# Performance work log

Hardware: AMD Instinct MI355X
Metric: run time of the kernel (lower is better)

The kernel has to match this reference:

```python
import jax, jax.numpy as jnp
import numpy as np

B, C = 8388608, 4
OTHERS_IDX = 3

def setup_inputs() -> dict:
    key = jax.random.key(0)
    k1, k2 = jax.random.split(key)
    preds = jax.random.normal(k1, (B, C), dtype=jnp.float32)
    target = jax.random.randint(k2, (B,), 0, C, dtype=jnp.int64)
    return {"preds": preds, "target": target, "others_idx": OTHERS_IDX}

def reference(preds, target, others_idx):
    # softmax over class dim (dim=1 in the torch module)
    probs = jax.nn.softmax(preds, axis=1)              # [B, C]
    p_o = probs[:, others_idx]                          # [B]
    s = probs.sum(axis=1)                               # [B] (== 1, but computed as in original)
    # per-sample false-negative error (samples whose target IS the 'others' class)
    fne_i = 0.5 * ((s - p_o) ** 2 + (p_o - 1.0) ** 2)   # [B]
    # per-sample false-positive error (samples whose target is NOT 'others')
    fpe_i = 0.5 * ((-p_o) ** 2 + p_o ** 2)              # [B]
    is_others = (target == others_idx)                  # [B] bool
    fne_num = jnp.sum(is_others).astype(probs.dtype)
    fpe_num = jnp.sum(~is_others).astype(probs.dtype)
    fne = jnp.sum(jnp.where(is_others, fne_i, 0.0)) / fne_num
    fpe = jnp.sum(jnp.where(is_others, 0.0, fpe_i)) / fpe_num
    return fpe + fne
```

## Files before the change

### kernel.cpp

```cpp
#include <hip/hip_runtime.h>


#define BLOCK 256
#define ROWS 16

__device__ __forceinline__ void mfe_row(float4 x, int t, int o,
                                        float& fne_acc, float& fpe_acc,
                                        float& cnt_acc) {
    float m = fmaxf(fmaxf(x.x, x.y), fmaxf(x.z, x.w));
    float e0 = __expf(x.x - m);
    float e1 = __expf(x.y - m);
    float e2 = __expf(x.z - m);
    float e3 = __expf(x.w - m);
    float S = (e0 + e1) + (e2 + e3);
    float r = 1.0f / S;
    float p0 = e0 * r, p1 = e1 * r, p2 = e2 * r, p3 = e3 * r;
    float s = ((p0 + p1) + p2) + p3;
    float po = (o == 0) ? p0 : (o == 1) ? p1 : (o == 2) ? p2 : p3;

    float d1 = s - po;
    float d2 = po - 1.0f;
    float fne_i = 0.5f * (d1 * d1 + d2 * d2);
    float fpe_i = po * po;

    bool is_o = (t == o);
    fne_acc += is_o ? fne_i : 0.0f;
    fpe_acc += is_o ? 0.0f : fpe_i;
    cnt_acc += is_o ? 1.0f : 0.0f;
}

__global__ __launch_bounds__(BLOCK) void mfe_partial(
    const float4* __restrict__ preds,
    const int* __restrict__ target,
    const int* __restrict__ others_idx_p,
    float* __restrict__ fne_part,
    float* __restrict__ fpe_part,
    float* __restrict__ cnt_part,
    int n_rows)
{
    const int o = *others_idx_p;
    int tid = blockIdx.x * blockDim.x + threadIdx.x;
    int nth = gridDim.x * blockDim.x;

    float fne_acc = 0.0f, fpe_acc = 0.0f, cnt_acc = 0.0f;

    if (tid + (ROWS - 1) * nth < n_rows) {
        float4 x[ROWS];
        int    t[ROWS];
        #pragma unroll
        for (int k = 0; k < ROWS; ++k) x[k] = preds[tid + k * nth];
        #pragma unroll
        for (int k = 0; k < ROWS; ++k) t[k] = target[tid + k * nth];
        #pragma unroll
        for (int k = 0; k < ROWS; ++k)
            mfe_row(x[k], t[k], o, fne_acc, fpe_acc, cnt_acc);
    } else {
        for (int i = tid; i < n_rows; i += nth)
            mfe_row(preds[i], target[i], o, fne_acc, fpe_acc, cnt_acc);
    }

    #pragma unroll
    for (int off = 32; off > 0; off >>= 1) {
        fne_acc += __shfl_down(fne_acc, off, 64);
        fpe_acc += __shfl_down(fpe_acc, off, 64);
        cnt_acc += __shfl_down(cnt_acc, off, 64);
    }

    if ((threadIdx.x & 63) == 0) {
        int part = blockIdx.x * (BLOCK / 64) + (threadIdx.x >> 6);
        fne_part[part] = fne_acc;
        fpe_part[part] = fpe_acc;
        cnt_part[part] = cnt_acc;
    }
}

__global__ __launch_bounds__(1024) void mfe_final(
    const float* __restrict__ fne_part,
    const float* __restrict__ fpe_part,
    const float* __restrict__ cnt_part,
    int nparts, int n_rows, float* __restrict__ out)
{
    double fn = 0.0, fp = 0.0, c = 0.0;
    for (int i = threadIdx.x; i < nparts; i += blockDim.x) {
        fn += (double)fne_part[i];
        fp += (double)fpe_part[i];
        c  += (double)cnt_part[i];
    }
    #pragma unroll
    for (int off = 32; off > 0; off >>= 1) {
        fn += __shfl_down(fn, off, 64);
        fp += __shfl_down(fp, off, 64);
        c  += __shfl_down(c, off, 64);
    }
    __shared__ double s_fn[16], s_fp[16], s_c[16];
    int wave = threadIdx.x >> 6;
    int lane = threadIdx.x & 63;
    if (lane == 0) { s_fn[wave] = fn; s_fp[wave] = fp; s_c[wave] = c; }
    __syncthreads();

    if (threadIdx.x == 0) {
        double tfn = 0.0, tfp = 0.0, tc = 0.0;
        int nwaves = blockDim.x >> 6;
        for (int w = 0; w < nwaves; ++w) { tfn += s_fn[w]; tfp += s_fp[w]; tc += s_c[w]; }
        double fne_num = tc;
        double fpe_num = (double)n_rows - fne_num;
        double res = 0.0;
        if (fpe_num > 0.0) res += tfp / fpe_num;
        if (fne_num > 0.0) res += tfn / fne_num;
        out[0] = (float)res;
    }
}

extern "C" void kernel_launch(void* const* d_in, const int* in_sizes, int n_in,
                              void* d_out, int out_size, void* d_ws, size_t ws_size,
                              hipStream_t stream) {
    const float4* preds = (const float4*)d_in[0];
    const int* target = (const int*)d_in[1];
    const int* others_idx = (const int*)d_in[2];
    float* out = (float*)d_out;

    int n_rows = in_sizes[0] / 4;

    int grid = (n_rows + BLOCK * ROWS - 1) / (BLOCK * ROWS);
    int nparts = grid * (BLOCK / 64);

    float* fne_part = (float*)d_ws;
    float* fpe_part = fne_part + nparts;
    float* cnt_part = fpe_part + nparts;

    mfe_partial<<<grid, BLOCK, 0, stream>>>(preds, target, others_idx,
                                            fne_part, fpe_part, cnt_part, n_rows);
    mfe_final<<<1, 1024, 0, stream>>>(fne_part, fpe_part, cnt_part,
                                      nparts, n_rows, out);
}
```

Baseline: 224.0 us.

## Double-buffer row loads with nontemporal loads and larger blocks

Replaces the load-all-then-compute pattern with a two-stage software pipeline that prefetches the next chunk of four rows while computing the current one, separated by a scheduling barrier. Loads become nontemporal, and the block size grows from 256 to 1024 threads. The aim is fewer live registers and streaming loads that bypass caching. The risk is fewer bytes in flight per thread, and coarser blocks at the tail.

```diff
diff --git a/kernel.cpp b/kernel.cpp
--- a/kernel.cpp
+++ b/kernel.cpp
@@ -1,10 +1,14 @@
 #include <hip/hip_runtime.h>
 
 
-#define BLOCK 256
+#define BLOCK 1024
 #define ROWS 16
+#define CHUNK 4
+#define STAGES (ROWS / CHUNK)
 
-__device__ __forceinline__ void mfe_row(float4 x, int t, int o,
+typedef float vfloat4 __attribute__((ext_vector_type(4)));
+
+__device__ __forceinline__ void mfe_row(vfloat4 x, int t, int o,
                                         float& fne_acc, float& fpe_acc,
                                         float& cnt_acc) {
     float m = fmaxf(fmaxf(x.x, x.y), fmaxf(x.z, x.w));
@@ -30,7 +34,7 @@
 }
 
 __global__ __launch_bounds__(BLOCK) void mfe_partial(
-    const float4* __restrict__ preds,
+    const vfloat4* __restrict__ preds,
     const int* __restrict__ target,
     const int* __restrict__ others_idx_p,
     float* __restrict__ fne_part,
@@ -39,21 +43,39 @@
     int n_rows)
 {
     const int o = *others_idx_p;
-    int tid = blockIdx.x * blockDim.x + threadIdx.x;
-    int nth = gridDim.x * blockDim.x;
+    int tid = blockIdx.x * BLOCK + threadIdx.x;
+    int nth = gridDim.x * BLOCK;
 
     float fne_acc = 0.0f, fpe_acc = 0.0f, cnt_acc = 0.0f;
 
     if (tid + (ROWS - 1) * nth < n_rows) {
-        float4 x[ROWS];
-        int    t[ROWS];
+        vfloat4 xbuf[2][CHUNK];
+        int     tbuf[2][CHUNK];
+
         #pragma unroll
-        for (int k = 0; k < ROWS; ++k) x[k] = preds[tid + k * nth];
+        for (int k = 0; k < CHUNK; ++k) {
+            int i = tid + k * nth;
+            xbuf[0][k] = __builtin_nontemporal_load(&preds[i]);
+            tbuf[0][k] = __builtin_nontemporal_load(&target[i]);
+        }
+
         #pragma unroll
-        for (int k = 0; k < ROWS; ++k) t[k] = target[tid + k * nth];
-        #pragma unroll
-        for (int k = 0; k < ROWS; ++k)
-            mfe_row(x[k], t[k], o, fne_acc, fpe_acc, cnt_acc);
+        for (int s = 0; s < STAGES; ++s) {
+            int cur = s & 1;
+            int nxt = cur ^ 1;
+            if (s + 1 < STAGES) {
+                #pragma unroll
+                for (int k = 0; k < CHUNK; ++k) {
+                    int i = tid + ((s + 1) * CHUNK + k) * nth;
+                    xbuf[nxt][k] = __builtin_nontemporal_load(&preds[i]);
+                    tbuf[nxt][k] = __builtin_nontemporal_load(&target[i]);
+                }
+            }
+            __builtin_amdgcn_sched_barrier(0);
+            #pragma unroll
+            for (int k = 0; k < CHUNK; ++k)
+                mfe_row(xbuf[cur][k], tbuf[cur][k], o, fne_acc, fpe_acc, cnt_acc);
+        }
     } else {
         for (int i = tid; i < n_rows; i += nth)
             mfe_row(preds[i], target[i], o, fne_acc, fpe_acc, cnt_acc);
@@ -114,7 +136,7 @@
 extern "C" void kernel_launch(void* const* d_in, const int* in_sizes, int n_in,
                               void* d_out, int out_size, void* d_ws, size_t ws_size,
                               hipStream_t stream) {
-    const float4* preds = (const float4*)d_in[0];
+    const vfloat4* preds = (const vfloat4*)d_in[0];
     const int* target = (const int*)d_in[1];
     const int* others_idx = (const int*)d_in[2];
     float* out = (float*)d_out;
```

Result: faster. 206.5 us (-7.8%).
